# Kernel optimization log

Hardware: AMD Instinct MI355X
Metric: run time of the kernel (lower is better)

The kernel has to match this reference:

```python
import jax, jax.numpy as jnp
import numpy as np

NUM_NODES = 2048      # nodes per graph
N = 65536             # total nodes = 16 pairs * 2 graphs * 2048
E = 524288            # total edges
D = 128               # node_state_dim
ED = 64               # edge_encoded_dim
H = 256               # message_hidden_dim
M = 128               # message_dim
U = 256               # update_hidden_dim


def _mlp3(x, W1, b1, W2, b2, W3, b3):
    h = jax.nn.relu(x @ W1 + b1)
    h = jax.nn.relu(h @ W2 + b2)
    return h @ W3 + b3


def setup_inputs() -> dict:
    key = jax.random.key(0)
    ks = jax.random.split(key, 16)
    s = 0.02
    inp = {
        "node_states": jax.random.normal(ks[0], (N, D), jnp.float32),
        "edges": jax.random.normal(ks[1], (E, ED), jnp.float32),
        "vertices": jax.random.randint(ks[2], (E, 2), 0, N, jnp.int32),
        # message_encoder params
        "mW1": jax.random.normal(ks[3], (2 * D + ED, H), jnp.float32) * s,
        "mb1": jnp.zeros((H,), jnp.float32),
        "mW2": jax.random.normal(ks[4], (H, H), jnp.float32) * s,
        "mb2": jnp.zeros((H,), jnp.float32),
        "mW3": jax.random.normal(ks[5], (H, M), jnp.float32) * s,
        "mb3": jnp.zeros((M,), jnp.float32),
        # node_update params
        "uW1": jax.random.normal(ks[6], (D + M + D, U), jnp.float32) * s,
        "ub1": jnp.zeros((U,), jnp.float32),
        "uW2": jax.random.normal(ks[7], (U, U), jnp.float32) * s,
        "ub2": jnp.zeros((U,), jnp.float32),
        "uW3": jax.random.normal(ks[8], (U, D), jnp.float32) * s,
        "ub3": jnp.zeros((D,), jnp.float32),
    }
    return inp


def reference(node_states, edges, vertices,
              mW1, mb1, mW2, mb2, mW3, mb3,
              uW1, ub1, uW2, ub2, uW3, ub3):
    # gather endpoint states: [E, D] each
    nodes_i = node_states[vertices[:, 0]]
    nodes_j = node_states[vertices[:, 1]]
    # message MLP on [E, 2D+ED]
    messages = _mlp3(jnp.concatenate([nodes_i, nodes_j, edges], axis=1),
                     mW1, mb1, mW2, mb2, mW3, mb3)
    # scatter-add each message to BOTH endpoints (torch code repeats messages
    # twice and scatters by [v0; v1; arange] with zero padding for all nodes)
    summed = (jax.ops.segment_sum(messages, vertices[:, 0], num_segments=N)
              + jax.ops.segment_sum(messages, vertices[:, 1], num_segments=N))
    # cross-graph attention vectors: pairs of graphs, difference both ways
    paired = node_states.reshape(-1, 2, NUM_NODES, D)
    attention = jnp.concatenate([paired[:, 0] - paired[:, 1],
                                 paired[:, 1] - paired[:, 0]], axis=1).reshape(-1, D)
    upd_in = jnp.concatenate([node_states, summed, attention], axis=1)
    return _mlp3(upd_in, uW1, ub1, uW2, ub2, uW3, ub3)
```

## Files before the change

kernel.cpp:

```cpp
#include <hip/hip_runtime.h>

#define NNODES 65536
#define NEDGES 524288

typedef short bf16x8 __attribute__((ext_vector_type(8)));
typedef float f32x4 __attribute__((ext_vector_type(4)));

#define OF_MW1 0
#define OF_MW2 81920
#define OF_MW3 147456
#define OF_UW1 180224
#define OF_UW2 278528
#define OF_UW3 344064
#define WF_BYTES (376832 * 2)

#define WS_MSGS_BYTES ((size_t)NEDGES * 128 * 2)
#define WS_NSB_OFF    WS_MSGS_BYTES
#define WS_NSB_BYTES  ((size_t)NNODES * 128 * 2)
#define WS_EIDX_OFF   (WS_NSB_OFF + WS_NSB_BYTES)
#define WS_EIDX_BYTES ((size_t)NNODES * 64 * 4)
#define WS_CNT_OFF    (WS_EIDX_OFF + WS_EIDX_BYTES)
#define WS_CNT_BYTES  ((size_t)NNODES * 4)
#define WS_WF_OFF     (WS_CNT_OFF + WS_CNT_BYTES)
#define WS_NEED       (WS_WF_OFF + WF_BYTES)

#define WS_SUMMED_BYTES ((size_t)NNODES * 128 * 4)

__device__ __forceinline__ unsigned short f2bf(float x) {
  unsigned int u = __float_as_uint(x);
  return (unsigned short)((u + 0x7FFFu + ((u >> 16) & 1u)) >> 16);
}

__device__ __forceinline__ float bf2f(short s) {
  return __uint_as_float((unsigned int)(unsigned short)s << 16);
}

__device__ __forceinline__ unsigned int cvtpk(float a, float b) {
  unsigned int r;
  asm("v_cvt_pk_bf16_f32 %0, %1, %2" : "=v"(r) : "v"(a), "v"(b));
  return r;
}

__device__ __forceinline__ void cvt_store8(unsigned short* p, float4 a, float4 b) {
  *reinterpret_cast<uint4*>(p) =
      make_uint4(cvtpk(a.x, a.y), cvtpk(a.z, a.w), cvtpk(b.x, b.y), cvtpk(b.z, b.w));
}

template <int MT, int KT, int NTW>
__device__ __forceinline__ void gemm_tile(const unsigned short* A, const int lda,
                                          const unsigned short* Wf,
                                          f32x4 (&acc)[MT][NTW], const int lane) {
  const int ar = lane & 15;
  const int ak = (lane >> 4) << 3;
  bf16x8 bcur[NTW], acur[MT];
#pragma unroll
  for (int n = 0; n < NTW; ++n)
    bcur[n] = *reinterpret_cast<const bf16x8*>(&Wf[(size_t)(n * KT) * 512 + lane * 8]);
#pragma unroll
  for (int m = 0; m < MT; ++m)
    acur[m] = *reinterpret_cast<const bf16x8*>(&A[(m * 16 + ar) * lda + ak]);
#pragma unroll
  for (int kt = 0; kt < KT; ++kt) {
    bf16x8 bnxt[NTW], anxt[MT];
    if (kt + 1 < KT) {
#pragma unroll
      for (int n = 0; n < NTW; ++n)
        bnxt[n] = *reinterpret_cast<const bf16x8*>(
            &Wf[(size_t)(n * KT + kt + 1) * 512 + lane * 8]);
#pragma unroll
      for (int m = 0; m < MT; ++m)
        anxt[m] = *reinterpret_cast<const bf16x8*>(
            &A[(m * 16 + ar) * lda + (kt + 1) * 32 + ak]);
    }
#pragma unroll
    for (int n = 0; n < NTW; ++n)
#pragma unroll
      for (int m = 0; m < MT; ++m)
        acc[m][n] = __builtin_amdgcn_mfma_f32_16x16x32_bf16(acur[m], bcur[n], acc[m][n], 0, 0, 0);
    if (kt + 1 < KT) {
#pragma unroll
      for (int n = 0; n < NTW; ++n) bcur[n] = bnxt[n];
#pragma unroll
      for (int m = 0; m < MT; ++m) acur[m] = anxt[m];
    }
  }
}

template <int MT, int KT, int NTW>
__device__ __forceinline__ void gemm_tile_d2(const unsigned short* A, const int lda,
                                             const unsigned short* Wf,
                                             f32x4 (&acc)[MT][NTW], const int lane) {
  const int ar = lane & 15;
  const int ak = (lane >> 4) << 3;
  bf16x8 b[3][NTW];
  bf16x8 a2[2][MT];
#pragma unroll
  for (int n = 0; n < NTW; ++n)
    b[0][n] = *reinterpret_cast<const bf16x8*>(&Wf[(size_t)(n * KT) * 512 + lane * 8]);
  if constexpr (KT > 1) {
#pragma unroll
    for (int n = 0; n < NTW; ++n)
      b[1][n] = *reinterpret_cast<const bf16x8*>(&Wf[(size_t)(n * KT + 1) * 512 + lane * 8]);
  }
#pragma unroll
  for (int m = 0; m < MT; ++m)
    a2[0][m] = *reinterpret_cast<const bf16x8*>(&A[(m * 16 + ar) * lda + ak]);
#pragma unroll
  for (int kt = 0; kt < KT; ++kt) {
    if (kt + 2 < KT) {
#pragma unroll
      for (int n = 0; n < NTW; ++n)
        b[(kt + 2) % 3][n] = *reinterpret_cast<const bf16x8*>(
            &Wf[(size_t)(n * KT + kt + 2) * 512 + lane * 8]);
    }
    if (kt + 1 < KT) {
#pragma unroll
      for (int m = 0; m < MT; ++m)
        a2[(kt + 1) & 1][m] = *reinterpret_cast<const bf16x8*>(
            &A[(m * 16 + ar) * lda + (kt + 1) * 32 + ak]);
    }
#pragma unroll
    for (int n = 0; n < NTW; ++n)
#pragma unroll
      for (int m = 0; m < MT; ++m)
        acc[m][n] = __builtin_amdgcn_mfma_f32_16x16x32_bf16(a2[kt & 1][m], b[kt % 3][n],
                                                            acc[m][n], 0, 0, 0);
  }
}

__global__ void prep_weights(const float* __restrict__ mW1, const float* __restrict__ mW2,
                             const float* __restrict__ mW3, const float* __restrict__ uW1,
                             const float* __restrict__ uW2, const float* __restrict__ uW3,
                             unsigned short* __restrict__ wf) {
  const int f = blockIdx.x;
  const int lane = threadIdx.x;
  const float* W; int NC, KT, fl, base;
  if (f < 160)      { W = mW1; NC = 256; KT = 10; fl = f;       base = OF_MW1; }
  else if (f < 288) { W = mW2; NC = 256; KT = 8;  fl = f - 160; base = OF_MW2; }
  else if (f < 352) { W = mW3; NC = 128; KT = 8;  fl = f - 288; base = OF_MW3; }
  else if (f < 544) { W = uW1; NC = 256; KT = 12; fl = f - 352; base = OF_UW1; }
  else if (f < 672) { W = uW2; NC = 256; KT = 8;  fl = f - 544; base = OF_UW2; }
  else              { W = uW3; NC = 128; KT = 8;  fl = f - 672; base = OF_UW3; }
  const int n_t = fl / KT;
  const int k_t = fl % KT;
  const int col = n_t * 16 + (lane & 15);
  const int krow = k_t * 32 + ((lane >> 4) << 3);
  unsigned short* dst = wf + base + (size_t)fl * 512 + lane * 8;
#pragma unroll
  for (int e = 0; e < 8; ++e) dst[e] = f2bf(W[(size_t)(krow + e) * NC + col]);
}

__global__ void cvt_ns(const float* __restrict__ ns, unsigned short* __restrict__ nsb) {
  const size_t i = ((size_t)blockIdx.x * 256 + threadIdx.x) * 8;
  const float4* s = reinterpret_cast<const float4*>(ns + i);
  cvt_store8(&nsb[i], s[0], s[1]);
}

__global__ void fill_csr(const int* __restrict__ verts, int* __restrict__ cnt,
                         int* __restrict__ eidx) {
  const int k = blockIdx.x * 256 + threadIdx.x;
  const int v = verts[k];
  const int slot = atomicAdd(&cnt[v], 1);
  if (slot < 64) eidx[(size_t)v * 64 + slot] = k >> 1;
}

template <bool ATOMIC>
__global__ __launch_bounds__(256, 3) void msg_kernel(
    const float* __restrict__ ns, const unsigned short* __restrict__ nsb,
    const float* __restrict__ edg, const int* __restrict__ verts,
    const unsigned short* __restrict__ wf, const float* __restrict__ mb1,
    const float* __restrict__ mb2, const float* __restrict__ mb3,
    float* __restrict__ summed, unsigned short* __restrict__ msgs) {
  extern __shared__ unsigned short smem[];
  unsigned short* Xs = smem;

  const int tid = threadIdx.x;
  const int lane = tid & 63;
  const int w = tid >> 6;
  const int e0 = blockIdx.x * 64;

  {
    const int r = tid >> 4;
    const int c = (tid & 15) * 8;
#pragma unroll
    for (int p = 0; p < 4; ++p) {
      const int row = p * 16 + r;
      const int2 vv = *reinterpret_cast<const int2*>(&verts[(size_t)(e0 + row) * 2]);
      if constexpr (ATOMIC) {
        const float4* s0 = reinterpret_cast<const float4*>(ns + (size_t)vv.x * 128 + c);
        cvt_store8(&Xs[row * 328 + c], s0[0], s0[1]);
        const float4* s1 = reinterpret_cast<const float4*>(ns + (size_t)vv.y * 128 + c);
        cvt_store8(&Xs[row * 328 + 128 + c], s1[0], s1[1]);
      } else {
        *reinterpret_cast<bf16x8*>(&Xs[row * 328 + c]) =
            *reinterpret_cast<const bf16x8*>(&nsb[(size_t)vv.x * 128 + c]);
        *reinterpret_cast<bf16x8*>(&Xs[row * 328 + 128 + c]) =
            *reinterpret_cast<const bf16x8*>(&nsb[(size_t)vv.y * 128 + c]);
      }
    }
#pragma unroll
    for (int i = tid; i < 512; i += 256) {
      const int row = i >> 3;
      const int cc = (i & 7) * 8;
      const float4* s2 = reinterpret_cast<const float4*>(edg + (size_t)(e0 + row) * 64 + cc);
      cvt_store8(&Xs[row * 328 + 256 + cc], s2[0], s2[1]);
    }
  }
  __syncthreads();

  const int cw = lane & 15;
  const int rq = (lane >> 4) * 4;

  {
    f32x4 acc[4][4];
#pragma unroll
    for (int m = 0; m < 4; ++m)
#pragma unroll
      for (int n = 0; n < 4; ++n)
#pragma unroll
        for (int i = 0; i < 4; ++i) acc[m][n][i] = 0.0f;
    gemm_tile_d2<4, 10, 4>(Xs, 328, wf + OF_MW1 + (size_t)(w * 4) * 10 * 512, acc, lane);
    __syncthreads();
#pragma unroll
    for (int n = 0; n < 4; ++n) {
      const int col = w * 64 + n * 16 + cw;
      const float bias = mb1[col];
#pragma unroll
      for (int m = 0; m < 4; ++m)
#pragma unroll
        for (int q = 0; q < 4; ++q) {
          const int row = m * 16 + rq + q;
          Xs[row * 328 + col] = f2bf(fmaxf(acc[m][n][q] + bias, 0.0f));
        }
    }
  }
  __syncthreads();

  {
    f32x4 acc[4][4];
#pragma unroll
    for (int m = 0; m < 4; ++m)
#pragma unroll
      for (int n = 0; n < 4; ++n)
#pragma unroll
        for (int i = 0; i < 4; ++i) acc[m][n][i] = 0.0f;
    gemm_tile_d2<4, 8, 4>(Xs, 328, wf + OF_MW2 + (size_t)(w * 4) * 8 * 512, acc, lane);
    __syncthreads();
#pragma unroll
    for (int n = 0; n < 4; ++n) {
      const int col = w * 64 + n * 16 + cw;
      const float bias = mb2[col];
#pragma unroll
      for (int m = 0; m < 4; ++m)
#pragma unroll
        for (int q = 0; q < 4; ++q) {
          const int row = m * 16 + rq + q;
          Xs[row * 328 + col] = f2bf(fmaxf(acc[m][n][q] + bias, 0.0f));
        }
    }
  }
  __syncthreads();

  {
    f32x4 acc[4][2];
#pragma unroll
    for (int m = 0; m < 4; ++m)
#pragma unroll
      for (int n = 0; n < 2; ++n)
#pragma unroll
        for (int i = 0; i < 4; ++i) acc[m][n][i] = 0.0f;
    gemm_tile_d2<4, 8, 2>(Xs, 328, wf + OF_MW3 + (size_t)(w * 2) * 8 * 512, acc, lane);

    if constexpr (ATOMIC) {
#pragma unroll
      for (int n = 0; n < 2; ++n) {
        const int col = w * 32 + n * 16 + cw;
        const float bias = mb3[col];
#pragma unroll
        for (int m = 0; m < 4; ++m)
#pragma unroll
          for (int q = 0; q < 4; ++q) {
            const int row = m * 16 + rq + q;
            const int2 vv = *reinterpret_cast<const int2*>(&verts[(size_t)(e0 + row) * 2]);
            const float v = acc[m][n][q] + bias;
            unsafeAtomicAdd(&summed[(size_t)vv.x * 128 + col], v);
            unsafeAtomicAdd(&summed[(size_t)vv.y * 128 + col], v);
          }
      }
    } else {
#pragma unroll
      for (int n = 0; n < 2; ++n) {
        const int col = w * 32 + n * 16 + cw;
        const float bias = mb3[col];
#pragma unroll
        for (int m = 0; m < 4; ++m)
#pragma unroll
          for (int q = 0; q < 4; ++q) {
            const int row = m * 16 + rq + q;
            msgs[(size_t)(e0 + row) * 128 + col] = f2bf(acc[m][n][q] + bias);
          }
      }
    }
  }
}

template <bool GATHER>
__global__ __launch_bounds__(128, 3) void upd_kernel(
    const float* __restrict__ ns, const float* __restrict__ summed,
    const unsigned short* __restrict__ msgs, const int* __restrict__ cnt,
    const int* __restrict__ eidx, const unsigned short* __restrict__ wf,
    const float* __restrict__ ub1, const float* __restrict__ ub2,
    const float* __restrict__ ub3, float* __restrict__ out) {
  extern __shared__ unsigned short smem[];
  unsigned short* Xs = smem;

  const int tid = threadIdx.x;
  const int lane = tid & 63;
  const int w = tid >> 6;
  const int n0 = blockIdx.x * 32;

  for (int i = tid; i < 512; i += 128) {
    const int row = i >> 4;
    const int c = (i & 15) * 8;
    const int n = n0 + row;
    const float4* sA = reinterpret_cast<const float4*>(ns + (size_t)n * 128 + c);
    const float4 a0 = sA[0], a1 = sA[1];
    cvt_store8(&Xs[row * 392 + c], a0, a1);
    if constexpr (!GATHER) {
      const float4* sS = reinterpret_cast<const float4*>(summed + (size_t)n * 128 + c);
      cvt_store8(&Xs[row * 392 + 128 + c], sS[0], sS[1]);
    }
    const float4* sP = reinterpret_cast<const float4*>(ns + (size_t)(n ^ 2048) * 128 + c);
    const float4 p0 = sP[0], p1 = sP[1];
    float4 d0, d1;
    d0.x = a0.x - p0.x; d0.y = a0.y - p0.y; d0.z = a0.z - p0.z; d0.w = a0.w - p0.w;
    d1.x = a1.x - p1.x; d1.y = a1.y - p1.y; d1.z = a1.z - p1.z; d1.w = a1.w - p1.w;
    cvt_store8(&Xs[row * 392 + 256 + c], d0, d1);
  }

  if constexpr (GATHER) {
    for (int i = tid; i < 512; i += 128) {
      const int row = i >> 4;
      const int q4 = i & 15;
      reinterpret_cast<int4*>(&Xs[row * 392 + 128])[q4] =
          reinterpret_cast<const int4*>(&eidx[(size_t)(n0 + row) * 64])[q4];
    }
    __syncthreads();

    const int nl = tid >> 2;
    const int part = tid & 3;
    const int cn = min(cnt[n0 + nl], 64);
    const int* el = reinterpret_cast<const int*>(&Xs[nl * 392 + 128]);
    float acc[32];
#pragma unroll
    for (int k = 0; k < 32; ++k) acc[k] = 0.0f;
    for (int j = 0; j < cn; ++j) {
      const int e = el[j];
      const bf16x8* mp = reinterpret_cast<const bf16x8*>(&msgs[(size_t)e * 128 + part * 32]);
#pragma unroll
      for (int t = 0; t < 4; ++t) {
        const bf16x8 v = mp[t];
#pragma unroll
        for (int k = 0; k < 8; ++k) acc[t * 8 + k] += bf2f(v[k]);
      }
    }
    __syncthreads();
#pragma unroll
    for (int t = 0; t < 4; ++t) {
      *reinterpret_cast<uint4*>(&Xs[nl * 392 + 128 + part * 32 + t * 8]) =
          make_uint4(cvtpk(acc[t * 8 + 0], acc[t * 8 + 1]), cvtpk(acc[t * 8 + 2], acc[t * 8 + 3]),
                     cvtpk(acc[t * 8 + 4], acc[t * 8 + 5]), cvtpk(acc[t * 8 + 6], acc[t * 8 + 7]));
    }
  }
  __syncthreads();

  const int cw = lane & 15;
  const int rq = (lane >> 4) * 4;

  {
    f32x4 acc[2][8];
#pragma unroll
    for (int m = 0; m < 2; ++m)
#pragma unroll
      for (int n = 0; n < 8; ++n)
#pragma unroll
        for (int i = 0; i < 4; ++i) acc[m][n][i] = 0.0f;
    gemm_tile<2, 12, 8>(Xs, 392, wf + OF_UW1 + (size_t)(w * 8) * 12 * 512, acc, lane);
    __syncthreads();
#pragma unroll
    for (int n = 0; n < 8; ++n) {
      const int col = w * 128 + n * 16 + cw;
      const float bias = ub1[col];
#pragma unroll
      for (int m = 0; m < 2; ++m)
#pragma unroll
        for (int q = 0; q < 4; ++q) {
          const int row = m * 16 + rq + q;
          Xs[row * 392 + col] = f2bf(fmaxf(acc[m][n][q] + bias, 0.0f));
        }
    }
  }
  __syncthreads();

  {
    f32x4 acc[2][8];
#pragma unroll
    for (int m = 0; m < 2; ++m)
#pragma unroll
      for (int n = 0; n < 8; ++n)
#pragma unroll
        for (int i = 0; i < 4; ++i) acc[m][n][i] = 0.0f;
    gemm_tile<2, 8, 8>(Xs, 392, wf + OF_UW2 + (size_t)(w * 8) * 8 * 512, acc, lane);
    __syncthreads();
#pragma unroll
    for (int n = 0; n < 8; ++n) {
      const int col = w * 128 + n * 16 + cw;
      const float bias = ub2[col];
#pragma unroll
      for (int m = 0; m < 2; ++m)
#pragma unroll
        for (int q = 0; q < 4; ++q) {
          const int row = m * 16 + rq + q;
          Xs[row * 392 + col] = f2bf(fmaxf(acc[m][n][q] + bias, 0.0f));
        }
    }
  }
  __syncthreads();

  {
    f32x4 acc[2][4];
#pragma unroll
    for (int m = 0; m < 2; ++m)
#pragma unroll
      for (int n = 0; n < 4; ++n)
#pragma unroll
        for (int i = 0; i < 4; ++i) acc[m][n][i] = 0.0f;
    gemm_tile<2, 8, 4>(Xs, 392, wf + OF_UW3 + (size_t)(w * 4) * 8 * 512, acc, lane);
#pragma unroll
    for (int n = 0; n < 4; ++n) {
      const int col = w * 64 + n * 16 + cw;
      const float bias = ub3[col];
#pragma unroll
      for (int m = 0; m < 2; ++m)
#pragma unroll
        for (int q = 0; q < 4; ++q) {
          const int row = m * 16 + rq + q;
          out[(size_t)(n0 + row) * 128 + col] = acc[m][n][q] + bias;
        }
    }
  }
}

extern "C" void kernel_launch(void* const* d_in, const int* in_sizes, int n_in,
                              void* d_out, int out_size, void* d_ws, size_t ws_size,
                              hipStream_t stream) {
  const float* ns   = (const float*)d_in[0];
  const float* edg  = (const float*)d_in[1];
  const int* verts  = (const int*)d_in[2];
  const float* mW1  = (const float*)d_in[3];
  const float* mb1  = (const float*)d_in[4];
  const float* mW2  = (const float*)d_in[5];
  const float* mb2  = (const float*)d_in[6];
  const float* mW3  = (const float*)d_in[7];
  const float* mb3  = (const float*)d_in[8];
  const float* uW1  = (const float*)d_in[9];
  const float* ub1  = (const float*)d_in[10];
  const float* uW2  = (const float*)d_in[11];
  const float* ub2  = (const float*)d_in[12];
  const float* uW3  = (const float*)d_in[13];
  const float* ub3  = (const float*)d_in[14];
  float* out = (float*)d_out;

  const int msg_lds = 64 * 328 * 2;
  const int upd_lds = 32 * 392 * 2;

  if (ws_size >= WS_NEED) {
    unsigned short* msgs = (unsigned short*)d_ws;
    unsigned short* nsb  = (unsigned short*)((char*)d_ws + WS_NSB_OFF);
    int* eidx = (int*)((char*)d_ws + WS_EIDX_OFF);
    int* cnt  = (int*)((char*)d_ws + WS_CNT_OFF);
    unsigned short* wf = (unsigned short*)((char*)d_ws + WS_WF_OFF);

    (void)hipMemsetAsync(cnt, 0, WS_CNT_BYTES, stream);
    prep_weights<<<736, 64, 0, stream>>>(mW1, mW2, mW3, uW1, uW2, uW3, wf);
    cvt_ns<<<NNODES * 128 / 8 / 256, 256, 0, stream>>>(ns, nsb);
    fill_csr<<<2 * NEDGES / 256, 256, 0, stream>>>(verts, cnt, eidx);
    msg_kernel<false><<<NEDGES / 64, 256, msg_lds, stream>>>(
        ns, nsb, edg, verts, wf, mb1, mb2, mb3, nullptr, msgs);
    upd_kernel<true><<<NNODES / 32, 128, upd_lds, stream>>>(
        ns, nullptr, msgs, cnt, eidx, wf, ub1, ub2, ub3, out);
  } else {
    float* summed = (float*)d_ws;
    unsigned short* wf = (unsigned short*)((char*)d_ws + WS_SUMMED_BYTES);

    (void)hipMemsetAsync(summed, 0, WS_SUMMED_BYTES, stream);
    prep_weights<<<736, 64, 0, stream>>>(mW1, mW2, mW3, uW1, uW2, uW3, wf);
    msg_kernel<true><<<NEDGES / 64, 256, msg_lds, stream>>>(
        ns, nullptr, edg, verts, wf, mb1, mb2, mb3, summed, nullptr);
    upd_kernel<false><<<NNODES / 32, 128, upd_lds, stream>>>(
        ns, summed, nullptr, nullptr, nullptr, wf, ub1, ub2, ub3, out);
  }
}
```

Before: 460.4 us.

## Stage message-MLP inputs in MFMA fragment layout via direct global-to-LDS loads

Adds a new message kernel that keeps activations in LDS in MFMA-fragment order and gathers node and edge bf16 rows straight into LDS with global_load_lds. Edges are pre-converted to bf16 in a merged prep kernel that also absorbs the node conversion and CSR fill launches. The aim is to cut LDS footprint (allowing more blocks per CU), remove padded row-major reads, and drop launch overhead. The cost is an extra bf16 edge buffer written and read through global memory, and a path that depends on the workspace being large enough.

```diff
diff --git a/kernel.cpp b/kernel.cpp
--- a/kernel.cpp
+++ b/kernel.cpp
@@ -23,6 +23,9 @@
 #define WS_CNT_BYTES  ((size_t)NNODES * 4)
 #define WS_WF_OFF     (WS_CNT_OFF + WS_CNT_BYTES)
 #define WS_NEED       (WS_WF_OFF + WF_BYTES)
+#define WS_EB_OFF     WS_NEED
+#define WS_EB_BYTES   ((size_t)NEDGES * 64 * 2)
+#define WS_NEED2      (WS_EB_OFF + WS_EB_BYTES)
 
 #define WS_SUMMED_BYTES ((size_t)NNODES * 128 * 4)
 
@@ -44,6 +47,12 @@
 __device__ __forceinline__ void cvt_store8(unsigned short* p, float4 a, float4 b) {
   *reinterpret_cast<uint4*>(p) =
       make_uint4(cvtpk(a.x, a.y), cvtpk(a.z, a.w), cvtpk(b.x, b.y), cvtpk(b.z, b.w));
+}
+
+__device__ __forceinline__ void gload_lds16(const void* g, void* l) {
+  __builtin_amdgcn_global_load_lds(
+      (const __attribute__((address_space(1))) void*)g,
+      (__attribute__((address_space(3))) void*)l, 16, 0, 0);
 }
 
 template <int MT, int KT, int NTW>
@@ -87,44 +96,39 @@
 }
 
 template <int MT, int KT, int NTW>
-__device__ __forceinline__ void gemm_tile_d2(const unsigned short* A, const int lda,
-                                             const unsigned short* Wf,
-                                             f32x4 (&acc)[MT][NTW], const int lane) {
-  const int ar = lane & 15;
-  const int ak = (lane >> 4) << 3;
-  bf16x8 b[3][NTW];
-  bf16x8 a2[2][MT];
+__device__ __forceinline__ void gemm_tile_frag(const unsigned short* FB,
+                                               const unsigned short* Wf,
+                                               f32x4 (&acc)[MT][NTW], const int lane) {
+  bf16x8 bcur[NTW], acur[MT];
 #pragma unroll
   for (int n = 0; n < NTW; ++n)
-    b[0][n] = *reinterpret_cast<const bf16x8*>(&Wf[(size_t)(n * KT) * 512 + lane * 8]);
-  if constexpr (KT > 1) {
+    bcur[n] = *reinterpret_cast<const bf16x8*>(&Wf[(size_t)(n * KT) * 512 + lane * 8]);
+#pragma unroll
+  for (int m = 0; m < MT; ++m)
+    acur[m] = *reinterpret_cast<const bf16x8*>(&FB[(m * KT) * 512 + lane * 8]);
+#pragma unroll
+  for (int kt = 0; kt < KT; ++kt) {
+    bf16x8 bnxt[NTW], anxt[MT];
+    if (kt + 1 < KT) {
+#pragma unroll
+      for (int n = 0; n < NTW; ++n)
+        bnxt[n] = *reinterpret_cast<const bf16x8*>(
+            &Wf[(size_t)(n * KT + kt + 1) * 512 + lane * 8]);
+#pragma unroll
+      for (int m = 0; m < MT; ++m)
+        anxt[m] = *reinterpret_cast<const bf16x8*>(&FB[(m * KT + kt + 1) * 512 + lane * 8]);
+    }
 #pragma unroll
     for (int n = 0; n < NTW; ++n)
-      b[1][n] = *reinterpret_cast<const bf16x8*>(&Wf[(size_t)(n * KT + 1) * 512 + lane * 8]);
-  }
-#pragma unroll
-  for (int m = 0; m < MT; ++m)
-    a2[0][m] = *reinterpret_cast<const bf16x8*>(&A[(m * 16 + ar) * lda + ak]);
-#pragma unroll
-  for (int kt = 0; kt < KT; ++kt) {
-    if (kt + 2 < KT) {
-#pragma unroll
-      for (int n = 0; n < NTW; ++n)
-        b[(kt + 2) % 3][n] = *reinterpret_cast<const bf16x8*>(
-            &Wf[(size_t)(n * KT + kt + 2) * 512 + lane * 8]);
-    }
+#pragma unroll
+      for (int m = 0; m < MT; ++m)
+        acc[m][n] = __builtin_amdgcn_mfma_f32_16x16x32_bf16(acur[m], bcur[n], acc[m][n], 0, 0, 0);
     if (kt + 1 < KT) {
 #pragma unroll
-      for (int m = 0; m < MT; ++m)
-        a2[(kt + 1) & 1][m] = *reinterpret_cast<const bf16x8*>(
-            &A[(m * 16 + ar) * lda + (kt + 1) * 32 + ak]);
-    }
-#pragma unroll
-    for (int n = 0; n < NTW; ++n)
-#pragma unroll
-      for (int m = 0; m < MT; ++m)
-        acc[m][n] = __builtin_amdgcn_mfma_f32_16x16x32_bf16(a2[kt & 1][m], b[kt % 3][n],
-                                                            acc[m][n], 0, 0, 0);
+      for (int n = 0; n < NTW; ++n) bcur[n] = bnxt[n];
+#pragma unroll
+      for (int m = 0; m < MT; ++m) acur[m] = anxt[m];
+    }
   }
 }
 
@@ -150,18 +154,139 @@
   for (int e = 0; e < 8; ++e) dst[e] = f2bf(W[(size_t)(krow + e) * NC + col]);
 }
 
-__global__ void cvt_ns(const float* __restrict__ ns, unsigned short* __restrict__ nsb) {
-  const size_t i = ((size_t)blockIdx.x * 256 + threadIdx.x) * 8;
-  const float4* s = reinterpret_cast<const float4*>(ns + i);
-  cvt_store8(&nsb[i], s[0], s[1]);
-}
-
-__global__ void fill_csr(const int* __restrict__ verts, int* __restrict__ cnt,
-                         int* __restrict__ eidx) {
-  const int k = blockIdx.x * 256 + threadIdx.x;
-  const int v = verts[k];
-  const int slot = atomicAdd(&cnt[v], 1);
-  if (slot < 64) eidx[(size_t)v * 64 + slot] = k >> 1;
+__global__ void prep_all(const float* __restrict__ ns, unsigned short* __restrict__ nsb,
+                         const float* __restrict__ edg, unsigned short* __restrict__ eb,
+                         const int* __restrict__ verts, int* __restrict__ cnt,
+                         int* __restrict__ eidx, const int csr_base) {
+  const int b = blockIdx.x;
+  if (b < 4096) {
+    const size_t i = ((size_t)b * 256 + threadIdx.x) * 8;
+    const float4* s = reinterpret_cast<const float4*>(ns + i);
+    cvt_store8(&nsb[i], s[0], s[1]);
+  } else if (b < csr_base) {
+    const size_t i = ((size_t)(b - 4096) * 256 + threadIdx.x) * 8;
+    const float4* s = reinterpret_cast<const float4*>(edg + i);
+    cvt_store8(&eb[i], s[0], s[1]);
+  } else {
+    const int k = (b - csr_base) * 256 + threadIdx.x;
+    const int v = verts[k];
+    const int slot = atomicAdd(&cnt[v], 1);
+    if (slot < 64) eidx[(size_t)v * 64 + slot] = k >> 1;
+  }
+}
+
+__global__ __launch_bounds__(256, 4) void msg_frag_kernel(
+    const unsigned short* __restrict__ nsb, const unsigned short* __restrict__ eb,
+    const int* __restrict__ verts, const unsigned short* __restrict__ wf,
+    const float* __restrict__ mb1, const float* __restrict__ mb2,
+    const float* __restrict__ mb3, unsigned short* __restrict__ msgs) {
+  extern __shared__ unsigned short smem[];
+  unsigned short* FB = smem;
+
+  const int tid = threadIdx.x;
+  const int lane = tid & 63;
+  const int w = tid >> 6;
+  const int e0 = blockIdx.x * 64;
+
+  {
+    const int row = w * 16 + (lane & 15);
+    const int ko = (lane >> 4) << 3;
+    const int2 vv = *reinterpret_cast<const int2*>(&verts[(size_t)(e0 + row) * 2]);
+    const unsigned short* ni_p = nsb + (size_t)vv.x * 128 + ko;
+    const unsigned short* nj_p = nsb + (size_t)vv.y * 128 + ko;
+    const unsigned short* eg_p = eb + (size_t)(e0 + row) * 64 + ko;
+    unsigned short* fb_w = FB + w * 10 * 512;
+#pragma unroll
+    for (int kt = 0; kt < 4; ++kt)
+      gload_lds16(ni_p + kt * 32, fb_w + kt * 512);
+#pragma unroll
+    for (int kt = 0; kt < 4; ++kt)
+      gload_lds16(nj_p + kt * 32, fb_w + (4 + kt) * 512);
+#pragma unroll
+    for (int kt = 0; kt < 2; ++kt)
+      gload_lds16(eg_p + kt * 32, fb_w + (8 + kt) * 512);
+  }
+  __syncthreads();
+
+  const int cw = lane & 15;
+  const int rq = (lane >> 4) * 4;
+
+  {
+    f32x4 acc[4][4];
+#pragma unroll
+    for (int m = 0; m < 4; ++m)
+#pragma unroll
+      for (int n = 0; n < 4; ++n)
+#pragma unroll
+        for (int i = 0; i < 4; ++i) acc[m][n][i] = 0.0f;
+    gemm_tile_frag<4, 10, 4>(FB, wf + OF_MW1 + (size_t)(w * 4) * 10 * 512, acc, lane);
+    __syncthreads();
+#pragma unroll
+    for (int n = 0; n < 4; ++n) {
+      const int col = w * 64 + n * 16 + cw;
+      const float bias = mb1[col];
+      const int kt2 = col >> 5;
+      const int lb = ((col >> 3) & 3) << 4;
+      const int j = col & 7;
+#pragma unroll
+      for (int m = 0; m < 4; ++m)
+#pragma unroll
+        for (int q = 0; q < 4; ++q)
+          FB[(m * 8 + kt2) * 512 + (lb + rq + q) * 8 + j] =
+              f2bf(fmaxf(acc[m][n][q] + bias, 0.0f));
+    }
+  }
+  __syncthreads();
+
+  {
+    f32x4 acc[4][4];
+#pragma unroll
+    for (int m = 0; m < 4; ++m)
+#pragma unroll
+      for (int n = 0; n < 4; ++n)
+#pragma unroll
+        for (int i = 0; i < 4; ++i) acc[m][n][i] = 0.0f;
+    gemm_tile_frag<4, 8, 4>(FB, wf + OF_MW2 + (size_t)(w * 4) * 8 * 512, acc, lane);
+    __syncthreads();
+#pragma unroll
+    for (int n = 0; n < 4; ++n) {
+      const int col = w * 64 + n * 16 + cw;
+      const float bias = mb2[col];
+      const int kt2 = col >> 5;
+      const int lb = ((col >> 3) & 3) << 4;
+      const int j = col & 7;
+#pragma unroll
+      for (int m = 0; m < 4; ++m)
+#pragma unroll
+        for (int q = 0; q < 4; ++q)
+          FB[(m * 8 + kt2) * 512 + (lb + rq + q) * 8 + j] =
+              f2bf(fmaxf(acc[m][n][q] + bias, 0.0f));
+    }
+  }
+  __syncthreads();
+
+  {
+    f32x4 acc[4][2];
+#pragma unroll
+    for (int m = 0; m < 4; ++m)
+#pragma unroll
+      for (int n = 0; n < 2; ++n)
+#pragma unroll
+        for (int i = 0; i < 4; ++i) acc[m][n][i] = 0.0f;
+    gemm_tile_frag<4, 8, 2>(FB, wf + OF_MW3 + (size_t)(w * 2) * 8 * 512, acc, lane);
+#pragma unroll
+    for (int n = 0; n < 2; ++n) {
+      const int col = w * 32 + n * 16 + cw;
+      const float bias = mb3[col];
+#pragma unroll
+      for (int m = 0; m < 4; ++m)
+#pragma unroll
+        for (int q = 0; q < 4; ++q) {
+          const int row = m * 16 + rq + q;
+          msgs[(size_t)(e0 + row) * 128 + col] = f2bf(acc[m][n][q] + bias);
+        }
+    }
+  }
 }
 
 template <bool ATOMIC>
@@ -219,7 +344,7 @@
       for (int n = 0; n < 4; ++n)
 #pragma unroll
         for (int i = 0; i < 4; ++i) acc[m][n][i] = 0.0f;
-    gemm_tile_d2<4, 10, 4>(Xs, 328, wf + OF_MW1 + (size_t)(w * 4) * 10 * 512, acc, lane);
+    gemm_tile<4, 10, 4>(Xs, 328, wf + OF_MW1 + (size_t)(w * 4) * 10 * 512, acc, lane);
     __syncthreads();
 #pragma unroll
     for (int n = 0; n < 4; ++n) {
@@ -244,7 +369,7 @@
       for (int n = 0; n < 4; ++n)
 #pragma unroll
         for (int i = 0; i < 4; ++i) acc[m][n][i] = 0.0f;
-    gemm_tile_d2<4, 8, 4>(Xs, 328, wf + OF_MW2 + (size_t)(w * 4) * 8 * 512, acc, lane);
+    gemm_tile<4, 8, 4>(Xs, 328, wf + OF_MW2 + (size_t)(w * 4) * 8 * 512, acc, lane);
     __syncthreads();
 #pragma unroll
     for (int n = 0; n < 4; ++n) {
@@ -269,7 +394,7 @@
       for (int n = 0; n < 2; ++n)
 #pragma unroll
         for (int i = 0; i < 4; ++i) acc[m][n][i] = 0.0f;
-    gemm_tile_d2<4, 8, 2>(Xs, 328, wf + OF_MW3 + (size_t)(w * 2) * 8 * 512, acc, lane);
+    gemm_tile<4, 8, 2>(Xs, 328, wf + OF_MW3 + (size_t)(w * 2) * 8 * 512, acc, lane);
 
     if constexpr (ATOMIC) {
 #pragma unroll
@@ -471,8 +596,9 @@
   const float* ub3  = (const float*)d_in[14];
   float* out = (float*)d_out;
 
-  const int msg_lds = 64 * 328 * 2;
-  const int upd_lds = 32 * 392 * 2;
+  const int frag_lds = 4 * 10 * 512 * 2;
+  const int msg_lds  = 64 * 328 * 2;
+  const int upd_lds  = 32 * 392 * 2;
 
   if (ws_size >= WS_NEED) {
     unsigned short* msgs = (unsigned short*)d_ws;
@@ -480,13 +606,19 @@
     int* eidx = (int*)((char*)d_ws + WS_EIDX_OFF);
     int* cnt  = (int*)((char*)d_ws + WS_CNT_OFF);
     unsigned short* wf = (unsigned short*)((char*)d_ws + WS_WF_OFF);
+    const bool has_eb = ws_size >= WS_NEED2;
+    unsigned short* eb = has_eb ? (unsigned short*)((char*)d_ws + WS_EB_OFF) : nullptr;
+    const int csr_base = has_eb ? 20480 : 4096;
 
     (void)hipMemsetAsync(cnt, 0, WS_CNT_BYTES, stream);
     prep_weights<<<736, 64, 0, stream>>>(mW1, mW2, mW3, uW1, uW2, uW3, wf);
-    cvt_ns<<<NNODES * 128 / 8 / 256, 256, 0, stream>>>(ns, nsb);
-    fill_csr<<<2 * NEDGES / 256, 256, 0, stream>>>(verts, cnt, eidx);
-    msg_kernel<false><<<NEDGES / 64, 256, msg_lds, stream>>>(
-        ns, nsb, edg, verts, wf, mb1, mb2, mb3, nullptr, msgs);
+    prep_all<<<csr_base + 4096, 256, 0, stream>>>(ns, nsb, edg, eb, verts, cnt, eidx, csr_base);
+    if (has_eb)
+      msg_frag_kernel<<<NEDGES / 64, 256, frag_lds, stream>>>(
+          nsb, eb, verts, wf, mb1, mb2, mb3, msgs);
+    else
+      msg_kernel<false><<<NEDGES / 64, 256, msg_lds, stream>>>(
+          ns, nsb, edg, verts, wf, mb1, mb2, mb3, nullptr, msgs);
     upd_kernel<true><<<NNODES / 32, 128, upd_lds, stream>>>(
         ns, nullptr, msgs, cnt, eidx, wf, ub1, ub2, ub3, out);
   } else {
```

Result: slower. 544.3 us (+18.2%).
